# Performance work log

Hardware: AMD Instinct MI355X
Metric: run time of the kernel (lower is better)

Reference implementation:

```python
import jax, jax.numpy as jnp
import numpy as np
from jax import lax

EPS = 1e-5
N_CROPS = 501
CROP_W = 500
RF = 65          # temporal receptive field
KS = 15          # conv1 kernel size
POOL = 3


def _bn(x, g, b, m, v, axis=1):
    shp = [1] * x.ndim
    shp[axis] = -1
    inv = g.reshape(shp) / jnp.sqrt(v.reshape(shp) + EPS)
    return (x - m.reshape(shp)) * inv + b.reshape(shp)


def setup_inputs() -> dict:
    key = jax.random.key(0)
    ks = jax.random.split(key, 16)
    B, C_IN, CH, T = 16, 1, 22, 1001
    F = 36
    OUT = 4
    FLAT = F * 43  # 1548 (corrected fc in_features; repo constant 504 is inconsistent)
    d = {
        "x": jax.random.normal(ks[0], (B, C_IN, CH, T), jnp.float32),
        # temporal conv [1,65]
        "w_t": jax.random.normal(ks[1], (F, 1, 1, RF), jnp.float32) * 0.1,
        "b_t": jax.random.normal(ks[2], (F,), jnp.float32) * 0.1,
        "bn_t_g": jax.random.uniform(ks[3], (F,), jnp.float32, 0.5, 1.5),
        "bn_t_b": jax.random.normal(ks[4], (F,), jnp.float32) * 0.1,
        "bn_t_m": jax.random.normal(ks[5], (F,), jnp.float32) * 0.1,
        "bn_t_v": jax.random.uniform(ks[6], (F,), jnp.float32, 0.5, 1.5),
        # spatial conv [22,1]
        "w_s": jax.random.normal(ks[7], (F, F, CH, 1), jnp.float32) * 0.05,
        "b_s": jax.random.normal(ks[8], (F,), jnp.float32) * 0.1,
        "bn_s_g": jax.random.uniform(ks[9], (F,), jnp.float32, 0.5, 1.5),
        "bn_s_b": jax.random.normal(ks[10], (F,), jnp.float32) * 0.1,
        "bn_s_m": jax.random.normal(ks[11], (F,), jnp.float32) * 0.1,
        "bn_s_v": jax.random.uniform(ks[12], (F,), jnp.float32, 0.5, 1.5),
        # conv1 [1,15] (as 1-D conv over time)
        "w_c": jax.random.normal(ks[13], (F, F, KS), jnp.float32) * 0.05,
        "b_c": jax.random.normal(ks[14], (F,), jnp.float32) * 0.1,
        "bn_c_g": jnp.ones((F,), jnp.float32),
        "bn_c_b": jnp.zeros((F,), jnp.float32),
        "bn_c_m": jnp.zeros((F,), jnp.float32),
        "bn_c_v": jnp.ones((F,), jnp.float32),
        # fc
        "w_fc": jax.random.normal(ks[15], (OUT, FLAT), jnp.float32) * 0.02,
        "b_fc": jnp.zeros((OUT,), jnp.float32),
    }
    return d


def reference(x, w_t, b_t, bn_t_g, bn_t_b, bn_t_m, bn_t_v,
              w_s, b_s, bn_s_g, bn_s_b, bn_s_m, bn_s_v,
              w_c, b_c, bn_c_g, bn_c_b, bn_c_m, bn_c_v,
              w_fc, b_fc):
    B = x.shape[0]
    F = w_t.shape[0]
    OUT = b_fc.shape[0]

    # temporal + spatial conv/BN/ELU are shift-invariant -> compute once over full T
    h = lax.conv_general_dilated(x, w_t, (1, 1), 'VALID',
                                 dimension_numbers=('NCHW', 'OIHW', 'NCHW'))
    h = h + b_t[None, :, None, None]                       # [B,36,22,937]
    h = jax.nn.elu(_bn(h, bn_t_g, bn_t_b, bn_t_m, bn_t_v))
    h = lax.conv_general_dilated(h, w_s, (1, 1), 'VALID',
                                 dimension_numbers=('NCHW', 'OIHW', 'NCHW'))
    h = h + b_s[None, :, None, None]                       # [B,36,1,937]
    h = jax.nn.elu(_bn(h, bn_s_g, bn_s_b, bn_s_m, bn_s_v))
    h = h[:, :, 0, :]                                      # [B,36,937]

    TW = CROP_W - RF + 1  # 436: temporal width of each crop after temporal conv

    def crop_logits(i):
        sl = lax.dynamic_slice_in_dim(h, i, TW, axis=2)    # [B,36,436]
        p1 = sl[:, :, :435].reshape(B, F, 145, POOL).mean(-1)  # avgpool1 -> [B,36,145]
        c = lax.conv_general_dilated(p1, w_c, (1,), 'VALID',
                                     dimension_numbers=('NCH', 'OIH', 'NCH'))
        c = c + b_c[None, :, None]                          # [B,36,131]
        c = jax.nn.elu(_bn(c, bn_c_g, bn_c_b, bn_c_m, bn_c_v))
        p2 = c[:, :, :129].reshape(B, F, 43, POOL).mean(-1)  # avgpool2 -> [B,36,43]
        flat = p2.reshape(B, -1)                            # [B,1548]
        return flat @ w_fc.T + b_fc                         # [B,OUT]

    def step(acc, i):
        return acc + crop_logits(i), None

    init = jnp.zeros((B, OUT), x.dtype)
    total, _ = lax.scan(step, init, jnp.arange(N_CROPS))
    return total / N_CROPS
```

## Files before the change

kernel.cpp:

```cpp
#include <hip/hip_runtime.h>

#define EPS 1e-5f
#define B 16
#define CH 22
#define T_IN 1001
#define F 36
#define RF 65
#define T1 937
#define FC 792
#define KW 99
#define UN 885
#define PSPAN 304
#define KS 15
#define GN 295
#define WN 129
#define M43 43
#define BF 576
#define FLAT 1548

#define H2_OFF  0
#define EP_OFF  539712
#define WTT_OFF 4617792
#define WST_OFF 4620132
#define WCT_OFF 4648644
#define BN_OFF  4668084
#define H1_OFF  4668352

__device__ __forceinline__ float elu_f(float v) {
    return v > 0.f ? v : (__expf(v) - 1.f);
}

__global__ __launch_bounds__(256) void k_prep(
    const float* __restrict__ w_t, const float* __restrict__ w_s,
    const float* __restrict__ w_c,
    const float* __restrict__ b_t, const float* __restrict__ g_t,
    const float* __restrict__ be_t,const float* __restrict__ m_t,
    const float* __restrict__ v_t,
    const float* __restrict__ b_s, const float* __restrict__ g_s,
    const float* __restrict__ be_s,const float* __restrict__ m_s,
    const float* __restrict__ v_s,
    const float* __restrict__ b_c, const float* __restrict__ g_c,
    const float* __restrict__ be_c,const float* __restrict__ m_c,
    const float* __restrict__ v_c, const float* __restrict__ b_fc,
    float* __restrict__ wtT, float* __restrict__ wsT,
    float* __restrict__ wcT, float* __restrict__ bnz,
    float* __restrict__ out)
{
    int i = blockIdx.x * 256 + threadIdx.x;
    if (i < F * RF)     { int k = i / F,  fi = i % F; wtT[i] = w_t[fi * RF + k]; }
    if (i < FC * F)     { int fc = i / F, fo = i % F; wsT[i] = w_s[fo * FC + fc]; }
    if (i < F * KS * F) { int fk = i / F, fo = i % F; int f = fk / KS, k = fk % KS;
                          wcT[i] = w_c[(fo * F + f) * KS + k]; }
    if (i < F) {
        float s1 = g_t[i] * rsqrtf(v_t[i] + EPS);
        bnz[i]          = s1;
        bnz[F + i]      = (b_t[i] - m_t[i]) * s1 + be_t[i];
        float s2 = g_s[i] * rsqrtf(v_s[i] + EPS);
        bnz[2 * F + i]  = s2;
        bnz[3 * F + i]  = (b_s[i] - m_s[i]) * s2 + be_s[i];
        float s3 = g_c[i] * rsqrtf(v_c[i] + EPS);
        bnz[4 * F + i]  = s3;
        bnz[5 * F + i]  = (b_c[i] - m_c[i]) * s3 + be_c[i];
    }
    if (i < B * 4) out[i] = b_fc[i & 3];
}

__global__ __launch_bounds__(256) void k_tconv(
    const float* __restrict__ x, const float* __restrict__ wtT,
    const float* __restrict__ bnz, float* __restrict__ h1,
    int t_base, int TS, int TSeff)
{
    const int tloc = blockIdx.x * 256 + threadIdx.x;
    const int b = blockIdx.z, ch = blockIdx.y;
    int t = t_base + tloc;
    int tc = t < (T1 - 1) ? t : (T1 - 1);
    const float* xp = x + (b * CH + ch) * T_IN + tc;

    float acc[F];
    #pragma unroll
    for (int j = 0; j < F; ++j) acc[j] = 0.f;

    #pragma unroll 13
    for (int k = 0; k < RF; ++k) {
        float xv = xp[k];
        const float* wr = wtT + k * F;
        #pragma unroll
        for (int j = 0; j < F; ++j) acc[j] += xv * wr[j];
    }

    if (tloc < TSeff) {
        #pragma unroll
        for (int j = 0; j < F; ++j) {
            float s1 = bnz[j], o1 = bnz[F + j];
            h1[((size_t)(b * F + j) * CH + ch) * TS + tloc] =
                elu_f(acc[j] * s1 + o1);
        }
    }
}

__global__ __launch_bounds__(512) void k_sconv(
    const float* __restrict__ h1, const float* __restrict__ wsT,
    const float* __restrict__ bnz, float* __restrict__ h2,
    int t_base, int TS, int TSeff)
{
    __shared__ float Ls[8 * F * 64];
    const int tid = threadIdx.x;
    const int lane = tid & 63;
    const int w = __builtin_amdgcn_readfirstlane(tid >> 6);
    const int b = blockIdx.y;
    const int tl0 = blockIdx.x * 64;
    int tl = tl0 + lane;
    int tlc = tl < (TSeff - 1) ? tl : (TSeff - 1);

    const float* hq = h1 + ((size_t)b * FC + w * KW) * TS + tlc;
    const float* wb = wsT + (w * KW) * F;

    float acc[F];
    #pragma unroll
    for (int j = 0; j < F; ++j) acc[j] = 0.f;

    #pragma unroll 9
    for (int fc = 0; fc < KW; ++fc) {
        float hv = hq[(size_t)fc * TS];
        const float* wr = wb + fc * F;
        #pragma unroll
        for (int j = 0; j < F; ++j) acc[j] += hv * wr[j];
    }

    #pragma unroll
    for (int j = 0; j < F; ++j) Ls[(w * F + j) * 64 + lane] = acc[j];
    __syncthreads();

    for (int i = tid; i < F * 64; i += 512) {
        float s = 0.f;
        #pragma unroll
        for (int wq = 0; wq < 8; ++wq) s += Ls[wq * (F * 64) + i];
        int fo = i >> 6;
        int tloc2 = tl0 + (i & 63);
        int tg = t_base + tloc2;
        if (tloc2 < TSeff) {
            float s2 = bnz[2 * F + fo], o2 = bnz[3 * F + fo];
            h2[(b * F + fo) * T1 + tg] = elu_f(s * s2 + o2);
        }
    }
}

__global__ __launch_bounds__(256) void k_qconv(
    const float* __restrict__ h2, const float* __restrict__ wcT,
    float* __restrict__ Ep)
{
    __shared__ float Ps[5 * PSPAN];
    const int tid = threadIdx.x;
    const int slice = blockIdx.y, b = blockIdx.z;
    const int u0 = blockIdx.x * 256;
    const int f_base = slice < 4 ? slice * 5 : 20 + (slice - 4) * 4;
    const int nf     = slice < 4 ? 5 : 4;

    for (int i = tid; i < nf * PSPAN; i += 256) {
        int fl = i / PSPAN, j = i % PSPAN;
        const float* hr = h2 + (size_t)(b * F + f_base + fl) * T1;
        int s = u0 + j;
        int s0 = s     < T1 - 1 ? s     : T1 - 1;
        int s1 = s + 1 < T1 - 1 ? s + 1 : T1 - 1;
        int s2 = s + 2 < T1 - 1 ? s + 2 : T1 - 1;
        Ps[i] = (hr[s0] + hr[s1] + hr[s2]) * (1.f / 3.f);
    }
    __syncthreads();

    const int lu = tid;

    float acc[F];
    #pragma unroll
    for (int j = 0; j < F; ++j) acc[j] = 0.f;

    for (int fl = 0; fl < nf; ++fl) {
        const int pb = fl * PSPAN + lu;
        #pragma unroll 5
        for (int k = 0; k < KS; ++k) {
            float pv = Ps[pb + 3 * k];
            const float* wr = wcT + ((f_base + fl) * KS + k) * F;
            #pragma unroll
            for (int j = 0; j < F; ++j) acc[j] += pv * wr[j];
        }
    }

    int u_g = u0 + lu;
    if (u_g < UN) {
        #pragma unroll
        for (int j = 0; j < F; ++j)
            Ep[(((size_t)slice * B + b) * F + j) * UN + u_g] = acc[j];
    }
}

__global__ __launch_bounds__(256) void k_wins(
    const float* __restrict__ Ep, const float* __restrict__ bnz,
    const float* __restrict__ w_fc, float* __restrict__ out)
{
    __shared__ float Es[UN];
    __shared__ float G[GN];
    __shared__ float Ws[WN];
    __shared__ float Sm[M43];
    const int tid = threadIdx.x;
    const int bf = blockIdx.x;
    const int b = bf / F, f = bf % F;
    const float sc = bnz[4 * F + f];
    const float oc = bnz[5 * F + f];
    for (int i = tid; i < UN; i += 256) {
        float s = 0.f;
        #pragma unroll
        for (int sl = 0; sl < 8; ++sl)
            s += Ep[((size_t)sl * BF + bf) * UN + i];
        Es[i] = elu_f(s * sc + oc);
    }
    __syncthreads();
    for (int q = tid; q < GN; q += 256)
        G[q] = Es[3 * q] + Es[3 * q + 1] + Es[3 * q + 2];
    __syncthreads();
    if (tid < WN) {
        float a = 0.f;
        for (int q = tid; q < tid + 167; ++q) a += G[q];
        Ws[tid] = a;
    }
    __syncthreads();
    if (tid < M43)
        Sm[tid] = (Ws[3 * tid] + Ws[3 * tid + 1] + Ws[3 * tid + 2]) * (1.f / 3.f);
    __syncthreads();
    if (tid < 4) {
        const float* wr = w_fc + tid * FLAT + f * M43;
        float a = 0.f;
        #pragma unroll 43
        for (int m = 0; m < M43; ++m) a += Sm[m] * wr[m];
        atomicAdd(&out[b * 4 + tid], a * (1.f / 501.f));
    }
}

extern "C" void kernel_launch(void* const* d_in, const int* in_sizes, int n_in,
                              void* d_out, int out_size, void* d_ws, size_t ws_size,
                              hipStream_t stream) {
    const float* x    = (const float*)d_in[0];
    const float* w_t  = (const float*)d_in[1];
    const float* b_t  = (const float*)d_in[2];
    const float* g_t  = (const float*)d_in[3];
    const float* be_t = (const float*)d_in[4];
    const float* m_t  = (const float*)d_in[5];
    const float* v_t  = (const float*)d_in[6];
    const float* w_s  = (const float*)d_in[7];
    const float* b_s  = (const float*)d_in[8];
    const float* g_s  = (const float*)d_in[9];
    const float* be_s = (const float*)d_in[10];
    const float* m_s  = (const float*)d_in[11];
    const float* v_s  = (const float*)d_in[12];
    const float* w_c  = (const float*)d_in[13];
    const float* b_c  = (const float*)d_in[14];
    const float* g_c  = (const float*)d_in[15];
    const float* be_c = (const float*)d_in[16];
    const float* m_c  = (const float*)d_in[17];
    const float* v_c  = (const float*)d_in[18];
    const float* w_fc = (const float*)d_in[19];
    const float* b_fc = (const float*)d_in[20];

    float* ws  = (float*)d_ws;
    float* h2  = ws + H2_OFF;
    float* Ep  = ws + EP_OFF;
    float* wtT = ws + WTT_OFF;
    float* wsT = ws + WST_OFF;
    float* wcT = ws + WCT_OFF;
    float* bnz = ws + BN_OFF;
    float* h1  = ws + H1_OFF;
    float* out = (float*)d_out;

    long long availF = (long long)(ws_size / 4) - (long long)H1_OFF;
    long long tsl = availF / (B * FC);
    int TS;
    if (tsl >= T1) TS = T1;
    else { TS = (int)(tsl & ~63LL); if (TS < 64) TS = 64; }
    int nslab = (T1 + TS - 1) / TS;

    k_prep<<<dim3(112), 256, 0, stream>>>(
        w_t, w_s, w_c, b_t, g_t, be_t, m_t, v_t,
        b_s, g_s, be_s, m_s, v_s, b_c, g_c, be_c, m_c, v_c, b_fc,
        wtT, wsT, wcT, bnz, out);

    for (int sl = 0; sl < nslab; ++sl) {
        int t_base = sl * TS;
        int TSeff = T1 - t_base; if (TSeff > TS) TSeff = TS;
        k_tconv<<<dim3((TSeff + 255) / 256, CH, B), 256, 0, stream>>>(
            x, wtT, bnz, h1, t_base, TS, TSeff);
        k_sconv<<<dim3((TSeff + 63) / 64, B), 512, 0, stream>>>(
            h1, wsT, bnz, h2, t_base, TS, TSeff);
    }

    k_qconv<<<dim3(4, 8, B), 256, 0, stream>>>(h2, wcT, Ep);
    k_wins<<<dim3(BF), 256, 0, stream>>>(Ep, bnz, w_fc, out);
}
```

Baseline: 179.5 us.

## Fuse temporal and spatial convolutions into one kernel, dropping the h1 intermediate

Replaces the separate temporal-conv and spatial-conv kernels with a single k_front kernel. Each wave computes the temporal conv, BN and ELU for three input filters per channel in registers, then accumulates straight into the spatial conv outputs. The four partial sums are reduced through shared memory. This removes the large h1 buffer (B×792×937 floats), its global write and read, and the slab loop with its many launches. In exchange the grid shrinks to 240 blocks of 768 threads, and each thread holds 36 accumulators, which may underfill the GPU and limit latency hiding.

```diff
diff --git a/kernel.cpp b/kernel.cpp
--- a/kernel.cpp
+++ b/kernel.cpp
@@ -8,7 +8,8 @@
 #define RF 65
 #define T1 937
 #define FC 792
-#define KW 99
+#define TW 64
+#define NTW 15
 #define UN 885
 #define PSPAN 304
 #define KS 15
@@ -24,7 +25,6 @@
 #define WST_OFF 4620132
 #define WCT_OFF 4648644
 #define BN_OFF  4668084
-#define H1_OFF  4668352
 
 __device__ __forceinline__ float elu_f(float v) {
     return v > 0.f ? v : (__expf(v) - 1.f);
@@ -65,80 +65,74 @@
     if (i < B * 4) out[i] = b_fc[i & 3];
 }
 
-__global__ __launch_bounds__(256) void k_tconv(
+__global__ __launch_bounds__(768) void k_front(
     const float* __restrict__ x, const float* __restrict__ wtT,
-    const float* __restrict__ bnz, float* __restrict__ h1,
-    int t_base, int TS, int TSeff)
-{
-    const int tloc = blockIdx.x * 256 + threadIdx.x;
-    const int b = blockIdx.z, ch = blockIdx.y;
-    int t = t_base + tloc;
-    int tc = t < (T1 - 1) ? t : (T1 - 1);
-    const float* xp = x + (b * CH + ch) * T_IN + tc;
+    const float* __restrict__ wsT, const float* __restrict__ bnz,
+    float* __restrict__ h2)
+{
+    __shared__ float Ls[4 * F * TW];
+    const int tid = threadIdx.x;
+    const int lane = tid & 63;
+    const int w = __builtin_amdgcn_readfirstlane(tid >> 6);
+    const int fi0 = 3 * w;
+    const int b = blockIdx.y;
+    const int t0 = blockIdx.x * TW;
+    int t = t0 + lane;
+    int tc = t < T1 ? t : (T1 - 1);
 
     float acc[F];
     #pragma unroll
     for (int j = 0; j < F; ++j) acc[j] = 0.f;
 
-    #pragma unroll 13
-    for (int k = 0; k < RF; ++k) {
-        float xv = xp[k];
-        const float* wr = wtT + k * F;
-        #pragma unroll
-        for (int j = 0; j < F; ++j) acc[j] += xv * wr[j];
-    }
-
-    if (tloc < TSeff) {
-        #pragma unroll
-        for (int j = 0; j < F; ++j) {
-            float s1 = bnz[j], o1 = bnz[F + j];
-            h1[((size_t)(b * F + j) * CH + ch) * TS + tloc] =
-                elu_f(acc[j] * s1 + o1);
+    const float s10 = bnz[fi0],     o10 = bnz[F + fi0];
+    const float s11 = bnz[fi0 + 1], o11 = bnz[F + fi0 + 1];
+    const float s12 = bnz[fi0 + 2], o12 = bnz[F + fi0 + 2];
+
+    for (int ch = 0; ch < CH; ++ch) {
+        const float* xp = x + (b * CH + ch) * T_IN + tc;
+        float ha = 0.f, hb = 0.f, hc = 0.f;
+        #pragma unroll 13
+        for (int k = 0; k < RF; ++k) {
+            float xv = xp[k];
+            const float* wr = wtT + k * F + fi0;
+            ha += xv * wr[0];
+            hb += xv * wr[1];
+            hc += xv * wr[2];
         }
-    }
-}
-
-__global__ __launch_bounds__(512) void k_sconv(
-    const float* __restrict__ h1, const float* __restrict__ wsT,
-    const float* __restrict__ bnz, float* __restrict__ h2,
-    int t_base, int TS, int TSeff)
-{
-    __shared__ float Ls[8 * F * 64];
-    const int tid = threadIdx.x;
-    const int lane = tid & 63;
-    const int w = __builtin_amdgcn_readfirstlane(tid >> 6);
-    const int b = blockIdx.y;
-    const int tl0 = blockIdx.x * 64;
-    int tl = tl0 + lane;
-    int tlc = tl < (TSeff - 1) ? tl : (TSeff - 1);
-
-    const float* hq = h1 + ((size_t)b * FC + w * KW) * TS + tlc;
-    const float* wb = wsT + (w * KW) * F;
-
-    float acc[F];
-    #pragma unroll
-    for (int j = 0; j < F; ++j) acc[j] = 0.f;
-
-    #pragma unroll 9
-    for (int fc = 0; fc < KW; ++fc) {
-        float hv = hq[(size_t)fc * TS];
-        const float* wr = wb + fc * F;
-        #pragma unroll
-        for (int j = 0; j < F; ++j) acc[j] += hv * wr[j];
-    }
-
-    #pragma unroll
-    for (int j = 0; j < F; ++j) Ls[(w * F + j) * 64 + lane] = acc[j];
-    __syncthreads();
-
-    for (int i = tid; i < F * 64; i += 512) {
-        float s = 0.f;
-        #pragma unroll
-        for (int wq = 0; wq < 8; ++wq) s += Ls[wq * (F * 64) + i];
-        int fo = i >> 6;
-        int tloc2 = tl0 + (i & 63);
-        int tg = t_base + tloc2;
-        if (tloc2 < TSeff) {
+        float e0 = elu_f(ha * s10 + o10);
+        float e1 = elu_f(hb * s11 + o11);
+        float e2 = elu_f(hc * s12 + o12);
+        const float* w0 = wsT + ((fi0 + 0) * CH + ch) * F;
+        const float* w1 = wsT + ((fi0 + 1) * CH + ch) * F;
+        const float* w2 = wsT + ((fi0 + 2) * CH + ch) * F;
+        #pragma unroll
+        for (int fo = 0; fo < F; ++fo)
+            acc[fo] += e0 * w0[fo] + e1 * w1[fo] + e2 * w2[fo];
+    }
+
+    const int r = w & 3;
+    float* row = &Ls[(size_t)r * (F * TW)];
+    if (w < 4) {
+        #pragma unroll
+        for (int fo = 0; fo < F; ++fo) row[fo * TW + lane] = acc[fo];
+    }
+    __syncthreads();
+    if (w >= 4 && w < 8) {
+        #pragma unroll
+        for (int fo = 0; fo < F; ++fo) row[fo * TW + lane] += acc[fo];
+    }
+    __syncthreads();
+    if (w >= 8) {
+        #pragma unroll
+        for (int fo = 0; fo < F; ++fo) row[fo * TW + lane] += acc[fo];
+    }
+    __syncthreads();
+
+    for (int i = tid; i < F * TW; i += 768) {
+        float s = Ls[i] + Ls[F * TW + i] + Ls[2 * F * TW + i] + Ls[3 * F * TW + i];
+        int fo = i / TW, tl = i % TW;
+        int tg = t0 + tl;
+        if (tg < T1) {
             float s2 = bnz[2 * F + fo], o2 = bnz[3 * F + fo];
             h2[(b * F + fo) * T1 + tg] = elu_f(s * s2 + o2);
         }
@@ -266,30 +260,14 @@
     float* wsT = ws + WST_OFF;
     float* wcT = ws + WCT_OFF;
     float* bnz = ws + BN_OFF;
-    float* h1  = ws + H1_OFF;
     float* out = (float*)d_out;
-
-    long long availF = (long long)(ws_size / 4) - (long long)H1_OFF;
-    long long tsl = availF / (B * FC);
-    int TS;
-    if (tsl >= T1) TS = T1;
-    else { TS = (int)(tsl & ~63LL); if (TS < 64) TS = 64; }
-    int nslab = (T1 + TS - 1) / TS;
 
     k_prep<<<dim3(112), 256, 0, stream>>>(
         w_t, w_s, w_c, b_t, g_t, be_t, m_t, v_t,
         b_s, g_s, be_s, m_s, v_s, b_c, g_c, be_c, m_c, v_c, b_fc,
         wtT, wsT, wcT, bnz, out);
 
-    for (int sl = 0; sl < nslab; ++sl) {
-        int t_base = sl * TS;
-        int TSeff = T1 - t_base; if (TSeff > TS) TSeff = TS;
-        k_tconv<<<dim3((TSeff + 255) / 256, CH, B), 256, 0, stream>>>(
-            x, wtT, bnz, h1, t_base, TS, TSeff);
-        k_sconv<<<dim3((TSeff + 63) / 64, B), 512, 0, stream>>>(
-            h1, wsT, bnz, h2, t_base, TS, TSeff);
-    }
-
+    k_front<<<dim3(NTW, B), 768, 0, stream>>>(x, wtT, wsT, bnz, h2);
     k_qconv<<<dim3(4, 8, B), 256, 0, stream>>>(h2, wcT, Ep);
     k_wins<<<dim3(BF), 256, 0, stream>>>(Ep, bnz, w_fc, out);
 }
```

Measured after the change: 188.0 us. 1.05x slower.
